# Performance work log

Hardware: AMD Instinct MI355X
Metric: run time of the kernel (lower is better)

The kernel has to match this reference:

```python
import jax, jax.numpy as jnp
import numpy as np

N_TAU = 100  # steps per delay: dt = tau / N_TAU (backward code uses dt = 0.01*tau)


def F_model(x, y, t, W1, W2, b):
    # F(x(t), x(t - tau), t); t enters the signature but this Model is autonomous,
    # matching the repo's example models.
    return jnp.tanh(W1 @ x + W2 @ y + b)


def setup_inputs() -> dict:
    key = jax.random.key(0)
    d = 512
    k1, k2, k3, k4 = jax.random.split(key, 4)
    scale = 1.0 / np.sqrt(d).astype(np.float32)
    x_0 = jax.random.normal(k1, (d,), dtype=jnp.float32)
    W1 = jax.random.normal(k2, (d, d), dtype=jnp.float32) * scale
    W2 = jax.random.normal(k3, (d, d), dtype=jnp.float32) * scale
    b = jax.random.normal(k4, (d,), dtype=jnp.float32)
    tau = jnp.ones((), dtype=jnp.float32)  # time delay; dt = 0.01 * tau
    N = 2000  # = floor(T / dt) with T = 20, tau = 1
    return {"x_0": x_0, "tau": tau, "W1": W1, "W2": W2, "b": b, "N": N}


def reference(x_0, tau, W1, W2, b, N):
    """Forward-Euler DDE solve of x'(t) = F(x(t), x(t - tau), t), x(t) = x_0 for t <= 0.
    Returns the trajectory as a [d, N+1] array (kth column = state at step k),
    matching DDE_Solver's x_Trajectory layout."""
    d = x_0.shape[0]
    M = N_TAU + 1  # ring buffer holds the last N_tau+1 states
    dt = 0.01 * tau

    buf0 = jnp.zeros((d, M), dtype=x_0.dtype).at[:, 0].set(x_0)

    def step(buf, j):
        x_j = buf[:, j % M]
        # delayed state x(t_j - tau) = x_{j - N_tau}; (j - N_tau) % M == (j + 1) % M
        y_hist = buf[:, (j + 1) % M]
        y_j = jnp.where(j >= N_TAU, y_hist, x_0)  # pre-history: x(t) = x_0
        t_j = j * dt
        x_jp1 = x_j + dt * F_model(x_j, y_j, t_j, W1, W2, b)
        buf = buf.at[:, (j + 1) % M].set(x_jp1)
        return buf, x_jp1

    _, ys = jax.lax.scan(step, buf0, jnp.arange(N))  # ys: [N, d]
    return jnp.concatenate([x_0[:, None], ys.T], axis=1)  # [d, N+1]
```

## Files before the change

kernel.cpp:

```cpp
#include <hip/hip_runtime.h>


#define D     512
#define NTAU  100
#define M     112
#define HSLOT 101
#define NW    64

typedef unsigned long long u64;

__device__ __forceinline__ float lo_f(u64 v){ union{unsigned u; float f;} c; c.u=(unsigned)v; return c.f; }
__device__ __forceinline__ u64 pack_rec(unsigned tag, float x){ union{unsigned u; float f;} c; c.f=x; return ((u64)tag<<32)|(u64)c.u; }
__device__ __forceinline__ u64 ag_ld(const u64* p){
    return __hip_atomic_load(p, __ATOMIC_RELAXED, __HIP_MEMORY_SCOPE_AGENT);
}
__device__ __forceinline__ void ag_st(u64* p, u64 v){
    __hip_atomic_store(p, v, __ATOMIC_RELAXED, __HIP_MEMORY_SCOPE_AGENT);
}
__device__ __forceinline__ float sel8(const float* a, int k){
    float s = a[0];
    s = (k == 1) ? a[1] : s;  s = (k == 2) ? a[2] : s;
    s = (k == 3) ? a[3] : s;  s = (k == 4) ? a[4] : s;
    s = (k == 5) ? a[5] : s;  s = (k == 6) ? a[6] : s;
    s = (k == 7) ? a[7] : s;
    return s;
}

__global__ __launch_bounds__(64, 1) void ndde_r5(
    const float* __restrict__ x0p, const float* __restrict__ taup,
    const float* __restrict__ W1,  const float* __restrict__ W2,
    const float* __restrict__ bb,  const int* __restrict__ Np,
    float* __restrict__ out, u64* __restrict__ ring,
    float* __restrict__ hist, int use_hist)
{
    const int lane    = threadIdx.x & 63;
    const int wb      = blockIdx.x;
    const int rowbase = wb * 8;
    const int N       = Np[0];
    const float dt    = 0.01f * taup[0];

    float w1v[8][8], w2v[8][8];
    #pragma unroll
    for (int r = 0; r < 8; ++r){
        const float* p1 = W1 + (size_t)(rowbase + r) * D + lane;
        const float* p2 = W2 + (size_t)(rowbase + r) * D + lane;
        #pragma unroll
        for (int i = 0; i < 8; ++i){
            w1v[r][i] = p1[64 * i];
            w2v[r][i] = p2[64 * i];
        }
    }
    #pragma unroll
    for (int r = 0; r < 8; ++r){
        #pragma unroll
        for (int i = 0; i < 8; ++i)
            asm volatile("" : "+v"(w1v[r][i]), "+v"(w2v[r][i]));
    }

    float xv0[8];
    #pragma unroll
    for (int i = 0; i < 8; ++i) xv0[i] = x0p[64 * i + lane];
    float yp[8], a[8];
    #pragma unroll
    for (int r = 0; r < 8; ++r){
        float sy = 0.f, st = 0.f;
        #pragma unroll
        for (int i = 0; i < 8; ++i){
            sy = fmaf(w2v[r][i], xv0[i], sy);
            st = fmaf(w1v[r][i], xv0[i], st);
        }
        yp[r] = sy; a[r] = st + sy;
    }
    #pragma unroll
    for (int off = 32; off >= 1; off >>= 1){
        #pragma unroll
        for (int r = 0; r < 8; ++r) a[r] += __shfl_xor(a[r], off, 64);
    }

    float xloc = 0.f, bval = 0.f;
    if (lane < 8){
        const int row = rowbase + lane;
        xloc = x0p[row];
        bval = bb[row];
        out[(size_t)row * (N + 1)] = xloc;
        if (N >= 1){
            const float x1 = xloc + dt * tanhf(sel8(a, lane) + bval);
            xloc = x1;
            ag_st(ring + D + row, pack_rec(2u, x1));
            out[(size_t)row * (N + 1) + 1] = x1;
        }
    }

    float* myh = hist + (size_t)wb * HSLOT * D;

    u64 xr[8];
    float xf[8];
    int sx = 1, sp = 2, syr = 1;
    int hw = 0, hr = 0;
    bool dead = false;

    for (int j = 1; j < N && !dead; ++j){
        const bool needy  = (j > NTAU);
        const unsigned tx = (unsigned)(j + 1);
        const u64* px = ring + (size_t)sx * D + lane;

        u64 yr[8];
        if (!use_hist && needy){
            const u64* py = ring + (size_t)syr * D + lane;
            #pragma unroll
            for (int i = 0; i < 8; ++i) yr[i] = ag_ld(py + 64 * i);
        }

        int it = 0;
        for (;;){
            #pragma unroll
            for (int i = 0; i < 8; ++i) xr[i] = ag_ld(px + 64 * i);
            bool ok = true;
            #pragma unroll
            for (int i = 0; i < 8; ++i) ok &= ((unsigned)(xr[i] >> 32) == tx);
            if (__all(ok)) break;
            if (++it > (1 << 20)){ dead = true; break; }
        }
        #pragma unroll
        for (int i = 0; i < 8; ++i) xf[i] = lo_f(xr[i]);

        if (!use_hist && needy){
            const unsigned ty = (unsigned)(j - NTAU + 1);
            bool ok = true;
            #pragma unroll
            for (int i = 0; i < 8; ++i) ok &= ((unsigned)(yr[i] >> 32) == ty);
            if (!__all(ok)){
                const u64* py = ring + (size_t)syr * D + lane;
                int it2 = 0;
                for (;;){
                    #pragma unroll
                    for (int i = 0; i < 8; ++i) yr[i] = ag_ld(py + 64 * i);
                    bool ok2 = true;
                    #pragma unroll
                    for (int i = 0; i < 8; ++i) ok2 &= ((unsigned)(yr[i] >> 32) == ty);
                    if (__all(ok2)) break;
                    if (++it2 > (1 << 20)){ dead = true; break; }
                }
            }
            #pragma unroll
            for (int r = 0; r < 8; ++r){
                float sy = 0.f;
                #pragma unroll
                for (int i = 0; i < 8; ++i) sy = fmaf(w2v[r][i], lo_f(yr[i]), sy);
                yp[r] = sy;
            }
        }

        #pragma unroll
        for (int r = 0; r < 8; ++r){
            float s = yp[r];
            #pragma unroll
            for (int i = 0; i < 8; ++i) s = fmaf(w1v[r][i], xf[i], s);
            a[r] = s;
        }
        #pragma unroll
        for (int off = 32; off >= 1; off >>= 1){
            #pragma unroll
            for (int r = 0; r < 8; ++r) a[r] += __shfl_xor(a[r], off, 64);
        }
        if (lane < 8){
            const float xn = xloc + dt * tanhf(sel8(a, lane) + bval);
            xloc = xn;
            const int row = rowbase + lane;
            ag_st(ring + (size_t)sp * D + row, pack_rec(tx + 1, xn));
            out[(size_t)row * (N + 1) + (j + 1)] = xn;
        }

        if (use_hist){
            float* hwp = myh + (size_t)hw * D + lane;
            #pragma unroll
            for (int i = 0; i < 8; ++i) hwp[64 * i] = xf[i];
            if (j >= NTAU){
                const float* hrp = myh + (size_t)hr * D + lane;
                float yv[8];
                #pragma unroll
                for (int i = 0; i < 8; ++i) yv[i] = hrp[64 * i];
                #pragma unroll
                for (int r = 0; r < 8; ++r){
                    float sy = 0.f;
                    #pragma unroll
                    for (int i = 0; i < 8; ++i) sy = fmaf(w2v[r][i], yv[i], sy);
                    yp[r] = sy;
                }
                hr = (hr == HSLOT - 1) ? 0 : hr + 1;
            }
            hw = (hw == HSLOT - 1) ? 0 : hw + 1;
        }

        sx = (sx == M - 1) ? 0 : sx + 1;
        sp = (sp == M - 1) ? 0 : sp + 1;
        if (j >= NTAU + 1) syr = (syr == M - 1) ? 0 : syr + 1;
    }
}

extern "C" void kernel_launch(void* const* d_in, const int* in_sizes, int n_in,
                              void* d_out, int out_size, void* d_ws, size_t ws_size,
                              hipStream_t stream)
{
    const float* x0  = (const float*)d_in[0];
    const float* tau = (const float*)d_in[1];
    const float* W1  = (const float*)d_in[2];
    const float* W2  = (const float*)d_in[3];
    const float* b   = (const float*)d_in[4];
    const int*   Np  = (const int*)  d_in[5];

    const size_t ring_bytes = (size_t)M * D * 8;
    const size_t hist_bytes = (size_t)NW * HSLOT * D * 4;
    const int use_hist = (ws_size >= ring_bytes + hist_bytes) ? 1 : 0;

    u64*   ring = (u64*)d_ws;
    float* hist = (float*)((char*)d_ws + ring_bytes);

    hipLaunchKernelGGL(ndde_r5, dim3(NW), dim3(64), 0, stream,
                       x0, tau, W1, W2, b, Np, (float*)d_out, ring, hist, use_hist);
}
```

Measured before the change: 2.961 ms.

## Elect single-XCD workgroups and use sc0 non-atomic ring loads/stores

The kernel now launches 512 workgroups. Each reads its XCC ID, and the first XCD to gather 64 workgroups is elected to run the solver, so all inter-workgroup ring traffic stays within one XCD's L2. It then runs a token self-test to check that sc0-cached loads and stores see each other's writes, and only then switches the spin-poll and record stores to inline asm with sc0 instead of agent-scope atomics. The aim is to cut the latency of each step's cross-workgroup handshake. The cost is a startup election, an extra memset, and reliance on the hardware's undocumented XCD placement behaviour, with a fallback to the atomic path if the test fails.

New measurement: 3.403 ms. +14.9%, slower.

```diff
diff --git a/kernel.cpp b/kernel.cpp
--- a/kernel.cpp
+++ b/kernel.cpp
@@ -6,16 +6,56 @@
 #define M     112
 #define HSLOT 101
 #define NW    64
+#define NLAUNCH 512
 
 typedef unsigned long long u64;
 
 __device__ __forceinline__ float lo_f(u64 v){ union{unsigned u; float f;} c; c.u=(unsigned)v; return c.f; }
 __device__ __forceinline__ u64 pack_rec(unsigned tag, float x){ union{unsigned u; float f;} c; c.f=x; return ((u64)tag<<32)|(u64)c.u; }
+
 __device__ __forceinline__ u64 ag_ld(const u64* p){
     return __hip_atomic_load(p, __ATOMIC_RELAXED, __HIP_MEMORY_SCOPE_AGENT);
 }
 __device__ __forceinline__ void ag_st(u64* p, u64 v){
     __hip_atomic_store(p, v, __ATOMIC_RELAXED, __HIP_MEMORY_SCOPE_AGENT);
+}
+__device__ __forceinline__ int ag_ldi(const int* p){
+    return __hip_atomic_load(p, __ATOMIC_RELAXED, __HIP_MEMORY_SCOPE_AGENT);
+}
+__device__ __forceinline__ u64 ld1_fast(const u64* p){
+    u64 r;
+    asm volatile("global_load_dwordx2 %0, %1, off sc0\n\ts_waitcnt vmcnt(0)"
+                 : "=&v"(r) : "v"(p) : "memory");
+    return r;
+}
+
+template<bool FAST>
+__device__ __forceinline__ void rld8(const u64* p, u64 r[8]){
+    if (FAST){
+        asm volatile(
+            "global_load_dwordx2 %0, %8, off sc0\n\t"
+            "global_load_dwordx2 %1, %8, off offset:512 sc0\n\t"
+            "global_load_dwordx2 %2, %8, off offset:1024 sc0\n\t"
+            "global_load_dwordx2 %3, %8, off offset:1536 sc0\n\t"
+            "global_load_dwordx2 %4, %8, off offset:2048 sc0\n\t"
+            "global_load_dwordx2 %5, %8, off offset:2560 sc0\n\t"
+            "global_load_dwordx2 %6, %8, off offset:3072 sc0\n\t"
+            "global_load_dwordx2 %7, %8, off offset:3584 sc0\n\t"
+            "s_waitcnt vmcnt(0)"
+            : "=&v"(r[0]), "=&v"(r[1]), "=&v"(r[2]), "=&v"(r[3]),
+              "=&v"(r[4]), "=&v"(r[5]), "=&v"(r[6]), "=&v"(r[7])
+            : "v"(p) : "memory");
+    } else {
+        #pragma unroll
+        for (int i = 0; i < 8; ++i) r[i] = ag_ld(p + 64 * i);
+    }
+}
+template<bool FAST>
+__device__ __forceinline__ void st_rec(u64* p, u64 v){
+    if (FAST)
+        asm volatile("global_store_dwordx2 %0, %1, off sc0" :: "v"(p), "v"(v) : "memory");
+    else
+        ag_st(p, v);
 }
 __device__ __forceinline__ float sel8(const float* a, int k){
     float s = a[0];
@@ -26,73 +66,13 @@
     return s;
 }
 
-__global__ __launch_bounds__(64, 1) void ndde_r5(
-    const float* __restrict__ x0p, const float* __restrict__ taup,
-    const float* __restrict__ W1,  const float* __restrict__ W2,
-    const float* __restrict__ bb,  const int* __restrict__ Np,
-    float* __restrict__ out, u64* __restrict__ ring,
-    float* __restrict__ hist, int use_hist)
+template<bool FAST>
+__device__ __forceinline__ void run_loop(
+    int N, float dt, int lane, int rowbase,
+    float (&w1v)[8][8], float (&w2v)[8][8],
+    float (&yp)[8], float (&a)[8], float xloc, float bval,
+    u64* ring, float* myh, int use_hist, float* out)
 {
-    const int lane    = threadIdx.x & 63;
-    const int wb      = blockIdx.x;
-    const int rowbase = wb * 8;
-    const int N       = Np[0];
-    const float dt    = 0.01f * taup[0];
-
-    float w1v[8][8], w2v[8][8];
-    #pragma unroll
-    for (int r = 0; r < 8; ++r){
-        const float* p1 = W1 + (size_t)(rowbase + r) * D + lane;
-        const float* p2 = W2 + (size_t)(rowbase + r) * D + lane;
-        #pragma unroll
-        for (int i = 0; i < 8; ++i){
-            w1v[r][i] = p1[64 * i];
-            w2v[r][i] = p2[64 * i];
-        }
-    }
-    #pragma unroll
-    for (int r = 0; r < 8; ++r){
-        #pragma unroll
-        for (int i = 0; i < 8; ++i)
-            asm volatile("" : "+v"(w1v[r][i]), "+v"(w2v[r][i]));
-    }
-
-    float xv0[8];
-    #pragma unroll
-    for (int i = 0; i < 8; ++i) xv0[i] = x0p[64 * i + lane];
-    float yp[8], a[8];
-    #pragma unroll
-    for (int r = 0; r < 8; ++r){
-        float sy = 0.f, st = 0.f;
-        #pragma unroll
-        for (int i = 0; i < 8; ++i){
-            sy = fmaf(w2v[r][i], xv0[i], sy);
-            st = fmaf(w1v[r][i], xv0[i], st);
-        }
-        yp[r] = sy; a[r] = st + sy;
-    }
-    #pragma unroll
-    for (int off = 32; off >= 1; off >>= 1){
-        #pragma unroll
-        for (int r = 0; r < 8; ++r) a[r] += __shfl_xor(a[r], off, 64);
-    }
-
-    float xloc = 0.f, bval = 0.f;
-    if (lane < 8){
-        const int row = rowbase + lane;
-        xloc = x0p[row];
-        bval = bb[row];
-        out[(size_t)row * (N + 1)] = xloc;
-        if (N >= 1){
-            const float x1 = xloc + dt * tanhf(sel8(a, lane) + bval);
-            xloc = x1;
-            ag_st(ring + D + row, pack_rec(2u, x1));
-            out[(size_t)row * (N + 1) + 1] = x1;
-        }
-    }
-
-    float* myh = hist + (size_t)wb * HSLOT * D;
-
     u64 xr[8];
     float xf[8];
     int sx = 1, sp = 2, syr = 1;
@@ -107,19 +87,17 @@
         u64 yr[8];
         if (!use_hist && needy){
             const u64* py = ring + (size_t)syr * D + lane;
-            #pragma unroll
-            for (int i = 0; i < 8; ++i) yr[i] = ag_ld(py + 64 * i);
+            rld8<FAST>(py, yr);
         }
 
         int it = 0;
         for (;;){
-            #pragma unroll
-            for (int i = 0; i < 8; ++i) xr[i] = ag_ld(px + 64 * i);
+            rld8<FAST>(px, xr);
             bool ok = true;
             #pragma unroll
             for (int i = 0; i < 8; ++i) ok &= ((unsigned)(xr[i] >> 32) == tx);
             if (__all(ok)) break;
-            if (++it > (1 << 20)){ dead = true; break; }
+            if (++it > (1 << 21)){ dead = true; break; }
         }
         #pragma unroll
         for (int i = 0; i < 8; ++i) xf[i] = lo_f(xr[i]);
@@ -133,13 +111,12 @@
                 const u64* py = ring + (size_t)syr * D + lane;
                 int it2 = 0;
                 for (;;){
-                    #pragma unroll
-                    for (int i = 0; i < 8; ++i) yr[i] = ag_ld(py + 64 * i);
+                    rld8<FAST>(py, yr);
                     bool ok2 = true;
                     #pragma unroll
                     for (int i = 0; i < 8; ++i) ok2 &= ((unsigned)(yr[i] >> 32) == ty);
                     if (__all(ok2)) break;
-                    if (++it2 > (1 << 20)){ dead = true; break; }
+                    if (++it2 > (1 << 21)){ dead = true; break; }
                 }
             }
             #pragma unroll
@@ -167,7 +144,7 @@
             const float xn = xloc + dt * tanhf(sel8(a, lane) + bval);
             xloc = xn;
             const int row = rowbase + lane;
-            ag_st(ring + (size_t)sp * D + row, pack_rec(tx + 1, xn));
+            st_rec<FAST>(ring + (size_t)sp * D + row, pack_rec(tx + 1, xn));
             out[(size_t)row * (N + 1) + (j + 1)] = xn;
         }
 
@@ -198,6 +175,125 @@
     }
 }
 
+__global__ __launch_bounds__(64, 1) void ndde_r6(
+    const float* __restrict__ x0p, const float* __restrict__ taup,
+    const float* __restrict__ W1,  const float* __restrict__ W2,
+    const float* __restrict__ bb,  const int* __restrict__ Np,
+    float* __restrict__ out, int* __restrict__ ectl,
+    u64* __restrict__ ring, float* __restrict__ hist, int use_hist)
+{
+    const int lane = threadIdx.x & 63;
+
+    int xcd;
+    asm("s_getreg_b32 %0, hwreg(HW_REG_XCC_ID, 0, 4)" : "=s"(xcd));
+    xcd &= 7;
+    int rank = -1;
+    if (lane == 0){
+        int r = __hip_atomic_fetch_add(&ectl[8 + xcd], 1, __ATOMIC_RELAXED, __HIP_MEMORY_SCOPE_AGENT);
+        if (r < NW){
+            if (r == NW - 1){
+                int expv = 0;
+                __hip_atomic_compare_exchange_strong(&ectl[0], &expv, xcd + 1,
+                    __ATOMIC_RELAXED, __ATOMIC_RELAXED, __HIP_MEMORY_SCOPE_AGENT);
+            }
+            int w, g = 1 << 22;
+            do { w = ag_ldi(&ectl[0]); } while (w == 0 && --g);
+            if (w == xcd + 1) rank = r;
+        }
+    }
+    rank = __shfl(rank, 0, 64);
+    if (rank < 0) return;
+
+    u64* tst = (u64*)((char*)ectl + 1024);
+    if (lane == 0){
+        u64 tok = pack_rec(0x7E570000u | (unsigned)rank, 3.f);
+        asm volatile("global_store_dwordx2 %0, %1, off sc0" :: "v"(tst + rank), "v"(tok) : "memory");
+    }
+    bool myok = false;
+    for (int it = 0; it < 8192; ++it){
+        const u64 v = ld1_fast(tst + lane);
+        const bool ok = ((unsigned)(v >> 32)) == (0x7E570000u | (unsigned)lane);
+        if (__all(ok)){ myok = true; break; }
+    }
+    int dec = 0;
+    if (lane == 0){
+        if (myok) __hip_atomic_fetch_add(&ectl[33], 1, __ATOMIC_RELAXED, __HIP_MEMORY_SCOPE_AGENT);
+        __hip_atomic_fetch_add(&ectl[32], 1, __ATOMIC_RELAXED, __HIP_MEMORY_SCOPE_AGENT);
+        if (rank == 0){
+            int dn, g = 1 << 22;
+            do { dn = ag_ldi(&ectl[32]); } while (dn < NW && --g);
+            const int oc = ag_ldi(&ectl[33]);
+            __hip_atomic_store(&ectl[34], (dn == NW && oc == NW) ? 1 : 2,
+                               __ATOMIC_RELAXED, __HIP_MEMORY_SCOPE_AGENT);
+        }
+        int g2 = 1 << 22;
+        do { dec = ag_ldi(&ectl[34]); } while (dec == 0 && --g2);
+    }
+    dec = __shfl(dec, 0, 64);
+    const bool go = (dec == 1);
+
+    const int rowbase = rank * 8;
+    const int N       = Np[0];
+    const float dt    = 0.01f * taup[0];
+
+    float w1v[8][8], w2v[8][8];
+    #pragma unroll
+    for (int r = 0; r < 8; ++r){
+        const float* p1 = W1 + (size_t)(rowbase + r) * D + lane;
+        const float* p2 = W2 + (size_t)(rowbase + r) * D + lane;
+        #pragma unroll
+        for (int i = 0; i < 8; ++i){
+            w1v[r][i] = p1[64 * i];
+            w2v[r][i] = p2[64 * i];
+        }
+    }
+    #pragma unroll
+    for (int r = 0; r < 8; ++r){
+        #pragma unroll
+        for (int i = 0; i < 8; ++i)
+            asm volatile("" : "+v"(w1v[r][i]), "+v"(w2v[r][i]));
+    }
+
+    float xv0[8];
+    #pragma unroll
+    for (int i = 0; i < 8; ++i) xv0[i] = x0p[64 * i + lane];
+    float yp[8], a[8];
+    #pragma unroll
+    for (int r = 0; r < 8; ++r){
+        float sy = 0.f, st = 0.f;
+        #pragma unroll
+        for (int i = 0; i < 8; ++i){
+            sy = fmaf(w2v[r][i], xv0[i], sy);
+            st = fmaf(w1v[r][i], xv0[i], st);
+        }
+        yp[r] = sy; a[r] = st + sy;
+    }
+    #pragma unroll
+    for (int off = 32; off >= 1; off >>= 1){
+        #pragma unroll
+        for (int r = 0; r < 8; ++r) a[r] += __shfl_xor(a[r], off, 64);
+    }
+
+    float xloc = 0.f, bval = 0.f;
+    if (lane < 8){
+        const int row = rowbase + lane;
+        xloc = x0p[row];
+        bval = bb[row];
+        out[(size_t)row * (N + 1)] = xloc;
+        if (N >= 1){
+            const float x1 = xloc + dt * tanhf(sel8(a, lane) + bval);
+            xloc = x1;
+            if (go) st_rec<true >(ring + D + row, pack_rec(2u, x1));
+            else    st_rec<false>(ring + D + row, pack_rec(2u, x1));
+            out[(size_t)row * (N + 1) + 1] = x1;
+        }
+    }
+
+    float* myh = hist + (size_t)rank * HSLOT * D;
+    if (go) run_loop<true >(N, dt, lane, rowbase, w1v, w2v, yp, a, xloc, bval, ring, myh, use_hist, out);
+    else    run_loop<false>(N, dt, lane, rowbase, w1v, w2v, yp, a, xloc, bval, ring, myh, use_hist, out);
+}
+
 extern "C" void kernel_launch(void* const* d_in, const int* in_sizes, int n_in,
                               void* d_out, int out_size, void* d_ws, size_t ws_size,
                               hipStream_t stream)
@@ -209,13 +305,16 @@
     const float* b   = (const float*)d_in[4];
     const int*   Np  = (const int*)  d_in[5];
 
+    const size_t ring_off   = 4096;
     const size_t ring_bytes = (size_t)M * D * 8;
     const size_t hist_bytes = (size_t)NW * HSLOT * D * 4;
-    const int use_hist = (ws_size >= ring_bytes + hist_bytes) ? 1 : 0;
-
-    u64*   ring = (u64*)d_ws;
-    float* hist = (float*)((char*)d_ws + ring_bytes);
-
-    hipLaunchKernelGGL(ndde_r5, dim3(NW), dim3(64), 0, stream,
-                       x0, tau, W1, W2, b, Np, (float*)d_out, ring, hist, use_hist);
-}
+    const int use_hist = (ws_size >= ring_off + ring_bytes + hist_bytes) ? 1 : 0;
+
+    hipMemsetAsync(d_ws, 0, 4096, stream);
+    int*   ectl = (int*)d_ws;
+    u64*   ring = (u64*)((char*)d_ws + ring_off);
+    float* hist = (float*)((char*)d_ws + ring_off + ring_bytes);
+
+    hipLaunchKernelGGL(ndde_r6, dim3(NLAUNCH), dim3(64), 0, stream,
+                       x0, tau, W1, W2, b, Np, (float*)d_out, ectl, ring, hist, use_hist);
+}
```

## Double-buffer spin-wait polling and shrink cross-lane reduction shuffles

Applied to the files above, without the earlier changes.

The spin-wait on the ring buffer now keeps two loads in flight, issuing the next batch of eight before checking the previous one, which aims to cut the time between a producer's write and the consumer seeing it. The 8-row butterfly reduction is restructured: each row is reduced across lanes 1, 2 and 4, one value per lane is selected, and that single value is reduced across lanes 8, 16 and 32, so fewer shuffles sit on the critical path. The asm register pins are removed and the launch attribute becomes waves_per_eu(1,1). This changes register pressure and adds extra polling memory traffic.

Measured after the change: 2.912 ms. About the same (-1.6%).

```diff
diff --git a/kernel.cpp b/kernel.cpp
--- a/kernel.cpp
+++ b/kernel.cpp
@@ -16,6 +16,16 @@
 }
 __device__ __forceinline__ void ag_st(u64* p, u64 v){
     __hip_atomic_store(p, v, __ATOMIC_RELAXED, __HIP_MEMORY_SCOPE_AGENT);
+}
+__device__ __forceinline__ void iss8(const u64* p, u64 r[8]){
+    #pragma unroll
+    for (int i = 0; i < 8; ++i) r[i] = ag_ld(p + 64 * i);
+}
+__device__ __forceinline__ bool chk8(const u64 r[8], unsigned t){
+    bool ok = true;
+    #pragma unroll
+    for (int i = 0; i < 8; ++i) ok &= ((unsigned)(r[i] >> 32) == t);
+    return __all(ok);
 }
 __device__ __forceinline__ float sel8(const float* a, int k){
     float s = a[0];
@@ -26,7 +36,9 @@
     return s;
 }
 
-__global__ __launch_bounds__(64, 1) void ndde_r5(
+__global__ __launch_bounds__(64)
+__attribute__((amdgpu_waves_per_eu(1, 1)))
+void ndde_r7(
     const float* __restrict__ x0p, const float* __restrict__ taup,
     const float* __restrict__ W1,  const float* __restrict__ W2,
     const float* __restrict__ bb,  const int* __restrict__ Np,
@@ -50,12 +62,6 @@
             w2v[r][i] = p2[64 * i];
         }
     }
-    #pragma unroll
-    for (int r = 0; r < 8; ++r){
-        #pragma unroll
-        for (int i = 0; i < 8; ++i)
-            asm volatile("" : "+v"(w1v[r][i]), "+v"(w2v[r][i]));
-    }
 
     float xv0[8];
     #pragma unroll
@@ -71,11 +77,18 @@
         }
         yp[r] = sy; a[r] = st + sy;
     }
-    #pragma unroll
-    for (int off = 32; off >= 1; off >>= 1){
-        #pragma unroll
-        for (int r = 0; r < 8; ++r) a[r] += __shfl_xor(a[r], off, 64);
-    }
+
+    const int sel = lane & 7;
+    #pragma unroll
+    for (int r = 0; r < 8; ++r){
+        a[r] += __shfl_xor(a[r], 1, 64);
+        a[r] += __shfl_xor(a[r], 2, 64);
+        a[r] += __shfl_xor(a[r], 4, 64);
+    }
+    float d0 = sel8(a, sel);
+    d0 += __shfl_xor(d0, 8, 64);
+    d0 += __shfl_xor(d0, 16, 64);
+    d0 += __shfl_xor(d0, 32, 64);
 
     float xloc = 0.f, bval = 0.f;
     if (lane < 8){
@@ -84,7 +97,7 @@
         bval = bb[row];
         out[(size_t)row * (N + 1)] = xloc;
         if (N >= 1){
-            const float x1 = xloc + dt * tanhf(sel8(a, lane) + bval);
+            const float x1 = xloc + dt * tanhf(d0 + bval);
             xloc = x1;
             ag_st(ring + D + row, pack_rec(2u, x1));
             out[(size_t)row * (N + 1) + 1] = x1;
@@ -93,7 +106,7 @@
 
     float* myh = hist + (size_t)wb * HSLOT * D;
 
-    u64 xr[8];
+    u64 xa[8], xb[8];
     float xf[8];
     int sx = 1, sp = 2, syr = 1;
     int hw = 0, hr = 0;
@@ -107,39 +120,34 @@
         u64 yr[8];
         if (!use_hist && needy){
             const u64* py = ring + (size_t)syr * D + lane;
-            #pragma unroll
-            for (int i = 0; i < 8; ++i) yr[i] = ag_ld(py + 64 * i);
-        }
-
+            iss8(py, yr);
+        }
+
+        iss8(px, xa);
         int it = 0;
         for (;;){
-            #pragma unroll
-            for (int i = 0; i < 8; ++i) xr[i] = ag_ld(px + 64 * i);
-            bool ok = true;
-            #pragma unroll
-            for (int i = 0; i < 8; ++i) ok &= ((unsigned)(xr[i] >> 32) == tx);
-            if (__all(ok)) break;
-            if (++it > (1 << 20)){ dead = true; break; }
-        }
-        #pragma unroll
-        for (int i = 0; i < 8; ++i) xf[i] = lo_f(xr[i]);
+            iss8(px, xb);
+            if (chk8(xa, tx)) break;
+            iss8(px, xa);
+            if (chk8(xb, tx)){
+                #pragma unroll
+                for (int i = 0; i < 8; ++i) xa[i] = xb[i];
+                break;
+            }
+            if ((it += 2) > (1 << 21)){ dead = true; break; }
+        }
+        #pragma unroll
+        for (int i = 0; i < 8; ++i) xf[i] = lo_f(xa[i]);
 
         if (!use_hist && needy){
             const unsigned ty = (unsigned)(j - NTAU + 1);
-            bool ok = true;
-            #pragma unroll
-            for (int i = 0; i < 8; ++i) ok &= ((unsigned)(yr[i] >> 32) == ty);
-            if (!__all(ok)){
+            if (!chk8(yr, ty)){
                 const u64* py = ring + (size_t)syr * D + lane;
                 int it2 = 0;
                 for (;;){
-                    #pragma unroll
-                    for (int i = 0; i < 8; ++i) yr[i] = ag_ld(py + 64 * i);
-                    bool ok2 = true;
-                    #pragma unroll
-                    for (int i = 0; i < 8; ++i) ok2 &= ((unsigned)(yr[i] >> 32) == ty);
-                    if (__all(ok2)) break;
-                    if (++it2 > (1 << 20)){ dead = true; break; }
+                    iss8(py, yr);
+                    if (chk8(yr, ty)) break;
+                    if (++it2 > (1 << 21)){ dead = true; break; }
                 }
             }
             #pragma unroll
@@ -159,12 +167,18 @@
             a[r] = s;
         }
         #pragma unroll
-        for (int off = 32; off >= 1; off >>= 1){
-            #pragma unroll
-            for (int r = 0; r < 8; ++r) a[r] += __shfl_xor(a[r], off, 64);
-        }
+        for (int r = 0; r < 8; ++r){
+            a[r] += __shfl_xor(a[r], 1, 64);
+            a[r] += __shfl_xor(a[r], 2, 64);
+            a[r] += __shfl_xor(a[r], 4, 64);
+        }
+        float dd = sel8(a, sel);
+        dd += __shfl_xor(dd, 8, 64);
+        dd += __shfl_xor(dd, 16, 64);
+        dd += __shfl_xor(dd, 32, 64);
+
         if (lane < 8){
-            const float xn = xloc + dt * tanhf(sel8(a, lane) + bval);
+            const float xn = xloc + dt * tanhf(dd + bval);
             xloc = xn;
             const int row = rowbase + lane;
             ag_st(ring + (size_t)sp * D + row, pack_rec(tx + 1, xn));
@@ -216,6 +230,6 @@
     u64*   ring = (u64*)d_ws;
     float* hist = (float*)((char*)d_ws + ring_bytes);
 
-    hipLaunchKernelGGL(ndde_r5, dim3(NW), dim3(64), 0, stream,
+    hipLaunchKernelGGL(ndde_r7, dim3(NW), dim3(64), 0, stream,
                        x0, tau, W1, W2, b, Np, (float*)d_out, ring, hist, use_hist);
 }
```
